# Performance work log

Measured on AMD Instinct MI355X. Metric: run time of the kernel, lower is better.

The kernel has to match this reference:

```python
import jax, jax.numpy as jnp
import numpy as np


def _conv(x, w, b, s):
    # x: NCHW, w: OIHW, VALID padding, stride s
    y = jax.lax.conv_general_dilated(x, w, (s, s), 'VALID',
                                     dimension_numbers=('NCHW', 'OIHW', 'NCHW'))
    return y + b[None, :, None, None]


def _deconv(x, w, b, s):
    # PyTorch ConvTranspose2d (weight IOHW, padding=0): conv of input dilated by s
    # with spatially-flipped, in/out-swapped kernel and full padding k-1.
    k = w.shape[2]
    wk = jnp.flip(w, (2, 3)).transpose(1, 0, 2, 3)  # -> OIHW
    y = jax.lax.conv_general_dilated(x, wk, (1, 1), [(k - 1, k - 1), (k - 1, k - 1)],
                                     lhs_dilation=(s, s),
                                     dimension_numbers=('NCHW', 'OIHW', 'NCHW'))
    return y + b[None, :, None, None]


def setup_inputs() -> dict:
    key = jax.random.key(0)
    ks = iter(jax.random.split(key, 40))
    def p(shape, scale=0.05):
        return jax.random.normal(next(ks), shape, jnp.float32) * scale
    return dict(
        x=jax.random.normal(next(ks), (50, 1, 64, 64), jnp.float32),
        action=jax.random.normal(next(ks), (50, 30), jnp.float32),
        h0=jax.random.normal(next(ks), (50, 1024), jnp.float32),
        c0=jax.random.normal(next(ks), (50, 1024), jnp.float32),
        conv1_w=p((32, 1, 4, 4)), conv1_b=p((32,)),
        conv2_w=p((64, 32, 4, 4)), conv2_b=p((64,)),
        conv3_w=p((128, 64, 4, 4)), conv3_b=p((128,)),
        conv4_w=p((256, 128, 4, 4)), conv4_b=p((256,)),
        fc1_w=p((482, 1024)), fc1_b=p((482,)),
        fc2_w=p((1024, 512)), fc2_b=p((1024,)),
        w_ih=p((4096, 1024)), w_hh=p((4096, 1024)),
        b_ih=p((4096,)), b_hh=p((4096,)),
        fcsd_w=p((1024, 1024)), fcsd_b=p((1024,)),
        d1_w=p((1024, 128, 5, 5)), d1_b=p((128,)),
        d2_w=p((128, 64, 5, 5)), d2_b=p((64,)),
        d3_w=p((64, 32, 6, 6)), d3_b=p((32,)),
        d4_w=p((32, 1, 6, 6)), d4_b=p((1,)),
        fc5_w=p((1, 512)), fc5_b=p((1,)),
    )


def reference(x, action, h0, c0,
              conv1_w, conv1_b, conv2_w, conv2_b, conv3_w, conv3_b, conv4_w, conv4_b,
              fc1_w, fc1_b, fc2_w, fc2_b,
              w_ih, w_hh, b_ih, b_hh,
              fcsd_w, fcsd_b,
              d1_w, d1_b, d2_w, d2_b, d3_w, d3_b, d4_w, d4_b,
              fc5_w, fc5_b):
    B = x.shape[0]  # 50 (hardcoded in original)
    T = 17          # PHYRE_MAX_TIMESTEPS
    h = x
    for w, b in ((conv1_w, conv1_b), (conv2_w, conv2_b), (conv3_w, conv3_b), (conv4_w, conv4_b)):
        h = jnp.tanh(_conv(h, w, b, 2))
    flat = h.reshape(B, -1)                      # [50, 1024]
    fc1 = flat @ fc1_w.T + fc1_b                 # [50, 482]
    z = jnp.concatenate([fc1, action], axis=1)   # [50, 512]
    fc2_out = jax.nn.leaky_relu(z @ fc2_w.T + fc2_b)  # [50, 1024]

    def step(carry, _):
        xt, hs, cs = carry
        g = xt @ w_ih.T + b_ih + hs @ w_hh.T + b_hh   # [B, 4096], gates i,f,g,o
        i, f, gg, o = jnp.split(g, 4, axis=1)
        cs = jax.nn.sigmoid(f) * cs + jax.nn.sigmoid(i) * jnp.tanh(gg)
        hs = jax.nn.sigmoid(o) * jnp.tanh(cs)
        return (hs, hs, cs), hs  # output fed back as next input

    _, outs = jax.lax.scan(step, (fc2_out, h0, c0), None, length=T)  # [17, 50, 1024]
    hd = jax.nn.leaky_relu(jnp.einsum('tbd,ed->tbe', outs, fcsd_w) + fcsd_b)
    hd = hd.reshape(T * B, 1024, 1, 1)  # t-major flatten, matching torch .view
    y = jnp.tanh(_deconv(hd, d1_w, d1_b, 2))   # [850,128,5,5]
    y = jnp.tanh(_deconv(y, d2_w, d2_b, 2))    # [850,64,13,13]
    y = jnp.tanh(_deconv(y, d3_w, d3_b, 2))    # [850,32,30,30]
    y = _deconv(y, d4_w, d4_b, 2)              # [850,1,64,64]
    obs = y.reshape(B, T, 1, 64, 64)  # faithful to original's view (layout quirk)
    reward = z @ fc5_w.T + fc5_b      # [50, 1]
    return obs, reward
```

## Files before the change

### kernel.cpp

```cpp
#include <hip/hip_runtime.h>
#include <math.h>

#define DI __device__ __forceinline__

DI float sigm(float x){ return 1.0f/(1.0f+expf(-x)); }
DI float lrelu(float x){ return x > 0.f ? x : 0.01f*x; }

template<int ACT>
DI float act_apply(float v){
    if (ACT == 1) return tanhf(v);
    if (ACT == 2) return lrelu(v);
    return v;
}

template<int CIN, int COUT>
__global__ __launch_bounds__(256)
void conv_enc_kernel(const float* __restrict__ in, const float* __restrict__ w,
                     const float* __restrict__ bias, float* __restrict__ out,
                     int N, int H, int OH)
{
    int idx = blockIdx.x*256 + threadIdx.x;
    int total = N*COUT*OH*OH;
    if (idx >= total) return;
    int ox = idx % OH; int t = idx / OH;
    int oy = t % OH;   t /= OH;
    int o  = t % COUT; int n = t / COUT;
    float acc = bias[o];
    const float* wp = w + o*CIN*16;
    const float* ip = in + ((size_t)n*CIN)*H*H + (oy*2)*H + ox*2;
    for (int c = 0; c < CIN; ++c) {
        const float* ipc = ip + c*H*H;
        const float* wpc = wp + c*16;
        #pragma unroll
        for (int ky = 0; ky < 4; ++ky)
            #pragma unroll
            for (int kx = 0; kx < 4; ++kx)
                acc = fmaf(ipc[ky*H + kx], wpc[ky*4 + kx], acc);
    }
    out[idx] = tanhf(acc);
}

template<int BM,int BN,int BK,bool BT,int ACT>
__global__ __launch_bounds__((BM/4)*(BN/4))
void gemm_kernel(const float* __restrict__ A, const float* __restrict__ Bm,
                 const float* __restrict__ bias, float* __restrict__ C,
                 int M, int N, int Kfull, int klen, int ldc, int bias_div,
                 long partStride)
{
    constexpr int TM = 4, TN = 4;
    constexpr int THREADS = (BM/TM)*(BN/TN);
    constexpr int LDA = BM + 4, LDB = BN + 4;
    __shared__ __align__(16) float As[BK][LDA];
    __shared__ __align__(16) float Bs[BK][LDB];
    int tid = threadIdx.x;
    int m0 = blockIdx.y * BM, n0 = blockIdx.x * BN;
    int koff = blockIdx.z * klen;
    C += (long)blockIdx.z * partStride;
    constexpr int NTX = BN/TN;
    int tx = tid % NTX, ty = tid / NTX;
    float acc[4][4];
    #pragma unroll
    for (int i=0;i<4;++i)
        #pragma unroll
        for (int j=0;j<4;++j) acc[i][j] = 0.f;

    for (int k0 = 0; k0 < klen; k0 += BK) {
        for (int e = tid; e < BM*BK; e += THREADS) {
            int k = e % BK, m = e / BK;
            As[k][m] = (m0+m < M) ? A[(size_t)(m0+m)*Kfull + koff + k0 + k] : 0.f;
        }
        if (BT) {
            for (int e = tid; e < BN*BK; e += THREADS) {
                int k = e % BK, n = e / BK;
                Bs[k][n] = (n0+n < N) ? Bm[(size_t)(n0+n)*Kfull + koff + k0 + k] : 0.f;
            }
        } else {
            for (int e = tid; e < BN*BK; e += THREADS) {
                int n = e % BN, k = e / BN;
                Bs[k][n] = (n0+n < N) ? Bm[(size_t)(koff + k0 + k)*N + n0+n] : 0.f;
            }
        }
        __syncthreads();
        #pragma unroll 8
        for (int k = 0; k < BK; ++k) {
            float4 a4 = *reinterpret_cast<const float4*>(&As[k][ty*4]);
            float4 b4 = *reinterpret_cast<const float4*>(&Bs[k][tx*4]);
            float av[4] = {a4.x, a4.y, a4.z, a4.w};
            float bv[4] = {b4.x, b4.y, b4.z, b4.w};
            #pragma unroll
            for (int i=0;i<4;++i)
                #pragma unroll
                for (int j=0;j<4;++j)
                    acc[i][j] = fmaf(av[i], bv[j], acc[i][j]);
        }
        __syncthreads();
    }
    #pragma unroll
    for (int i=0;i<4;++i) {
        int m = m0 + ty*4 + i;
        if (m >= M) continue;
        #pragma unroll
        for (int j=0;j<4;++j) {
            int n = n0 + tx*4 + j;
            if (n >= N) continue;
            float v = acc[i][j] + (bias ? bias[n / bias_div] : 0.f);
            C[(size_t)m*ldc + n] = act_apply<ACT>(v);
        }
    }
}

__global__ __launch_bounds__(256)
void addvec_kernel(const float* __restrict__ a, const float* __restrict__ b,
                   float* __restrict__ o, int n)
{
    int i = blockIdx.x*256 + threadIdx.x;
    if (i < n) o[i] = a[i] + b[i];
}

__global__ __launch_bounds__(64)
void concat_action_kernel(const float* __restrict__ action, float* __restrict__ z)
{
    int i = blockIdx.x*64 + threadIdx.x;
    if (i < 50*30) { int b = i/30, k = i%30; z[b*512 + 482 + k] = action[i]; }
}

__global__ __launch_bounds__(64)
void reward_kernel(const float* __restrict__ z, const float* __restrict__ w,
                   const float* __restrict__ b, float* __restrict__ out)
{
    int bi = threadIdx.x;
    if (bi < 50) {
        float acc = b[0];
        for (int k = 0; k < 512; ++k) acc = fmaf(z[bi*512 + k], w[k], acc);
        out[bi] = acc;
    }
}

__global__ __launch_bounds__(256)
void lstm_gates8_kernel(const float* __restrict__ gp, const float* __restrict__ bsum,
                        const float* __restrict__ c_prev,
                        float* __restrict__ c_out, float* __restrict__ h_out,
                        float* __restrict__ outs_t)
{
    int idx = blockIdx.x*256 + threadIdx.x;
    if (idx >= 50*1024) return;
    int b = idx >> 10, j = idx & 1023;
    float s0 = bsum[j], s1 = bsum[1024+j], s2 = bsum[2048+j], s3 = bsum[3072+j];
    #pragma unroll
    for (int p = 0; p < 8; ++p) {
        const float* base = gp + (size_t)p*204800 + b*4096 + j;
        s0 += base[0]; s1 += base[1024]; s2 += base[2048]; s3 += base[3072];
    }
    float cp = c_prev[idx];
    float c = sigm(s1)*cp + sigm(s0)*tanhf(s2);
    float h = sigm(s3)*tanhf(c);
    c_out[idx] = c; h_out[idx] = h; outs_t[idx] = h;
}

__global__ __launch_bounds__(256)
void wprep_kernel(const float* __restrict__ w, float* __restrict__ wp,
                  int CIN, int COUT, int KS)
{
    int idx = blockIdx.x*256 + threadIdx.x;
    int total = 4*CIN*COUT*12;
    if (idx >= total) return;
    int slot = idx % 12; int rem = idx / 12;
    int o = rem % COUT; rem /= COUT;
    int c = rem % CIN;  int pp = rem / CIN;
    int py = pp >> 1, px = pp & 1;
    int j = slot >> 2, i = slot & 3;
    int ky = py + 2*j, kx = px + 2*i;
    float v = 0.f;
    if (i < 3 && ky < KS && kx < KS)
        v = w[(((size_t)c*COUT + o)*KS + ky)*KS + kx];
    wp[idx] = v;
}

template<int CIN,int COUT,int HIN,int HOUT,int ACT,int VSPLIT,int ROWP,int TWU,
         int VPER,int TB,int MWAVES,int ISTR,int OSTR>
__global__ __launch_bounds__(256, MWAVES)
void deconv4_kernel(const float* __restrict__ in, const float* __restrict__ wp,
                    const float* __restrict__ bias, float* __restrict__ out)
{
    constexpr int NV = (HOUT + 1) / 2;
    constexpr int NVSEG = (NV + VSPLIT - 1) / VSPLIT;
    constexpr int NVB = (NVSEG + VPER - 1) / VPER;
    constexpr int ROWS_MAX = (NVSEG + 2 < HIN) ? (NVSEG + 2) : HIN;
    constexpr int NR4 = (TWU + 2 + 3) / 4;
    constexpr int RLEN = (TWU == 1) ? 4 : NR4*4;
    static_assert(NVB * COUT * TB <= 256, "tasks must fit one per thread");
    __shared__ __align__(16) float slab[CIN*ROWS_MAX*ROWP];

    int n   = blockIdx.x / VSPLIT;
    int seg = blockIdx.x % VSPLIT;
    int v0 = seg * NVSEG;
    int v1 = (v0 + NVSEG < NV) ? v0 + NVSEG : NV;
    int r0 = (v0 - 2 > 0) ? v0 - 2 : 0;
    int r1m = (v1 - 1 < HIN - 1) ? v1 - 1 : HIN - 1;
    int nrows = r1m - r0 + 1;
    int tid = threadIdx.x;
    const float* inb = in + (size_t)n*CIN*HIN*ISTR;
    const size_t PPSTR = (size_t)CIN*COUT*12;

    for (int e = tid; e < CIN*ROWS_MAX; e += 256) {
        int c = e / ROWS_MAX, ri = e % ROWS_MAX;
        if (ri < nrows) {
            const float* src = inb + ((size_t)c*HIN + r0 + ri)*ISTR;
            float* dst = slab + (c*ROWS_MAX + ri)*ROWP;
            dst[0] = 0.f; dst[1] = 0.f;
            #pragma unroll
            for (int x2 = HIN+2; x2 < ROWP; ++x2) dst[x2] = 0.f;
            for (int x2 = 0; x2 < HIN; ++x2) dst[2+x2] = src[x2];
        }
    }
    __syncthreads();

    int task = tid;
    int vi = task % NVB; int rem = task / NVB;
    int o = rem % COUT;  int tb = rem / COUT;
    int u0 = tb * TWU;
    bool anyv = false;
    int vg[VPER];
    #pragma unroll
    for (int q = 0; q < VPER; ++q) {
        vg[q] = v0 + vi + q*NVB;
        if (vg[q] < v1) anyv = true;
    }
    if (tb >= TB) anyv = false;

    float acc[VPER][2][2][TWU];
    #pragma unroll
    for (int q=0;q<VPER;++q)
        #pragma unroll
        for (int a=0;a<2;++a)
            #pragma unroll
            for (int b=0;b<2;++b)
                #pragma unroll
                for (int t=0;t<TWU;++t) acc[q][a][b][t] = 0.f;

    if (anyv) {
        const float* wb0 = wp + (size_t)o*12;
        for (int c = 0; c < CIN; ++c) {
            const float* wbase = wb0 + (size_t)c*COUT*12;
            const float* sc = slab + c*(ROWS_MAX*ROWP);
            #pragma unroll
            for (int jj = 0; jj < 3; ++jj) {
                float r[VPER][RLEN];
                #pragma unroll
                for (int q = 0; q < VPER; ++q) {
                    int iy = vg[q] - jj;
                    if (iy >= 0 && iy < HIN) {
                        const float* srow = sc + (iy - r0)*ROWP + u0;
                        if constexpr (TWU == 1) {
                            r[q][0] = srow[0]; r[q][1] = srow[1]; r[q][2] = srow[2];
                        } else {
                            #pragma unroll
                            for (int p4 = 0; p4 < NR4; ++p4) {
                                float4 f = *reinterpret_cast<const float4*>(srow + p4*4);
                                r[q][p4*4]=f.x; r[q][p4*4+1]=f.y; r[q][p4*4+2]=f.z; r[q][p4*4+3]=f.w;
                            }
                        }
                    } else {
                        #pragma unroll
                        for (int p4 = 0; p4 < RLEN; ++p4) r[q][p4] = 0.f;
                    }
                }
                #pragma unroll
                for (int pp = 0; pp < 4; ++pp) {
                    float4 w4 = *reinterpret_cast<const float4*>(wbase + pp*PPSTR + jj*4);
                    int py = pp >> 1, px = pp & 1;
                    #pragma unroll
                    for (int q = 0; q < VPER; ++q)
                        #pragma unroll
                        for (int t = 0; t < TWU; ++t)
                            acc[q][py][px][t] =
                                fmaf(w4.x, r[q][t+2],
                                fmaf(w4.y, r[q][t+1],
                                fmaf(w4.z, r[q][t], acc[q][py][px][t])));
                }
            }
        }
        float bv = bias[o];
        #pragma unroll
        for (int q = 0; q < VPER; ++q) {
            if (vg[q] >= v1) continue;
            #pragma unroll
            for (int py = 0; py < 2; ++py) {
                int y = py + 2*vg[q];
                if (y >= HOUT) continue;
                float* ob = out + (((size_t)n*COUT + o)*HOUT + y)*OSTR;
                #pragma unroll
                for (int t = 0; t < TWU; ++t) {
                    int x0 = 2*(u0+t);
                    if (x0 + 1 < HOUT) {
                        float2 qv;
                        qv.x = act_apply<ACT>(acc[q][py][0][t] + bv);
                        qv.y = act_apply<ACT>(acc[q][py][1][t] + bv);
                        *reinterpret_cast<float2*>(ob + x0) = qv;
                    } else if (x0 < HOUT) {
                        ob[x0] = act_apply<ACT>(acc[q][py][0][t] + bv);
                    }
                }
            }
        }
    }
}

extern "C" void kernel_launch(void* const* d_in, const int* in_sizes, int n_in,
                              void* d_out, int out_size, void* d_ws, size_t ws_size,
                              hipStream_t stream)
{
    const float* x       = (const float*)d_in[0];
    const float* action  = (const float*)d_in[1];
    const float* h0      = (const float*)d_in[2];
    const float* c0      = (const float*)d_in[3];
    const float* conv1_w = (const float*)d_in[4];  const float* conv1_b = (const float*)d_in[5];
    const float* conv2_w = (const float*)d_in[6];  const float* conv2_b = (const float*)d_in[7];
    const float* conv3_w = (const float*)d_in[8];  const float* conv3_b = (const float*)d_in[9];
    const float* conv4_w = (const float*)d_in[10]; const float* conv4_b = (const float*)d_in[11];
    const float* fc1_w   = (const float*)d_in[12]; const float* fc1_b   = (const float*)d_in[13];
    const float* fc2_w   = (const float*)d_in[14]; const float* fc2_b   = (const float*)d_in[15];
    const float* w_ih    = (const float*)d_in[16]; const float* w_hh    = (const float*)d_in[17];
    const float* b_ih    = (const float*)d_in[18]; const float* b_hh    = (const float*)d_in[19];
    const float* fcsd_w  = (const float*)d_in[20]; const float* fcsd_b  = (const float*)d_in[21];
    const float* d1_w    = (const float*)d_in[22]; const float* d1_b    = (const float*)d_in[23];
    const float* d2_w    = (const float*)d_in[24]; const float* d2_b    = (const float*)d_in[25];
    const float* d3_w    = (const float*)d_in[26]; const float* d3_b    = (const float*)d_in[27];
    const float* d4_w    = (const float*)d_in[28]; const float* d4_b    = (const float*)d_in[29];
    const float* fc5_w   = (const float*)d_in[30]; const float* fc5_b   = (const float*)d_in[31];
    float* out = (float*)d_out;
    float* ws  = (float*)d_ws;

    float* a1   = ws;
    float* a2   = a1 + 1537600;
    float* a3   = a2 + 627200;
    float* flat = a3 + 230400;
    float* z    = flat + 51200;
    float* fc2o = z + 25600;
    float* hbuf = fc2o + 51200;
    float* cbuf = hbuf + 51200;
    float* outs = cbuf + 51200;
    float* hd   = outs + 870400;
    float* wsum = hd + 870400;
    float* bsum = wsum + 4194304;
    float* wp2  = bsum + 4096;
    float* wp3  = wp2 + 393216;
    float* wp4  = wp3 + 98304;
    float* y1   = wp4 + 1536;
    float* y2   = y1 + 2720000;
    float* y3   = y2 + 11315200;
    float* g8   = y1;

    const int B = 50;
    const long GP = 204800;

    addvec_kernel<<<(4194304+255)/256, 256, 0, stream>>>(w_ih, w_hh, wsum, 4194304);
    addvec_kernel<<<(4096+255)/256, 256, 0, stream>>>(b_ih, b_hh, bsum, 4096);
    wprep_kernel<<<(4*128*64*12+255)/256, 256, 0, stream>>>(d2_w, wp2, 128, 64, 5);
    wprep_kernel<<<(4*64*32*12+255)/256, 256, 0, stream>>>(d3_w, wp3, 64, 32, 6);
    wprep_kernel<<<(4*32*1*12+255)/256, 256, 0, stream>>>(d4_w, wp4, 32, 1, 6);

    conv_enc_kernel<1,32><<<(B*32*31*31+255)/256, 256, 0, stream>>>(x, conv1_w, conv1_b, a1, B, 64, 31);
    conv_enc_kernel<32,64><<<(B*64*14*14+255)/256, 256, 0, stream>>>(a1, conv2_w, conv2_b, a2, B, 31, 14);
    conv_enc_kernel<64,128><<<(B*128*6*6+255)/256, 256, 0, stream>>>(a2, conv3_w, conv3_b, a3, B, 14, 6);
    conv_enc_kernel<128,256><<<(B*256*2*2+255)/256, 256, 0, stream>>>(a3, conv4_w, conv4_b, flat, B, 6, 2);

    {
        dim3 grid((482+63)/64, (B+31)/32, 1);
        gemm_kernel<32,64,32,true,0><<<grid, 128, 0, stream>>>(flat, fc1_w, fc1_b, z, B, 482, 1024, 1024, 512, 1, 0);
    }
    concat_action_kernel<<<(1500+63)/64, 64, 0, stream>>>(action, z);
    reward_kernel<<<1, 64, 0, stream>>>(z, fc5_w, fc5_b, out + (size_t)850*4096);

    {
        dim3 grid((1024+63)/64, (B+31)/32, 1);
        gemm_kernel<32,64,32,true,2><<<grid, 128, 0, stream>>>(z, fc2_w, fc2_b, fc2o, B, 1024, 512, 512, 1024, 1, 0);
    }

    {
        dim3 grid0(64, 2, 4);
        gemm_kernel<32,64,32,true,0><<<grid0, 128, 0, stream>>>(fc2o, w_ih, nullptr, g8, B, 4096, 1024, 256, 4096, 1, GP);
        gemm_kernel<32,64,32,true,0><<<grid0, 128, 0, stream>>>(h0, w_hh, nullptr, g8 + 4*GP, B, 4096, 1024, 256, 4096, 1, GP);
        lstm_gates8_kernel<<<200, 256, 0, stream>>>(g8, bsum, c0, cbuf, hbuf, outs);
        dim3 gridt(64, 2, 8);
        for (int t = 1; t < 17; ++t) {
            gemm_kernel<32,64,32,true,0><<<gridt, 128, 0, stream>>>(hbuf, wsum, nullptr, g8, B, 4096, 1024, 128, 4096, 1, GP);
            lstm_gates8_kernel<<<200, 256, 0, stream>>>(g8, bsum, cbuf, cbuf, hbuf, outs + (size_t)t*51200);
        }
    }

    {
        dim3 grid((1024+63)/64, (850+63)/64, 1);
        gemm_kernel<64,64,32,true,2><<<grid, 256, 0, stream>>>(outs, fcsd_w, fcsd_b, hd, 850, 1024, 1024, 1024, 1024, 1, 0);
    }
    {
        dim3 grid((3200+63)/64, (850+63)/64, 1);
        gemm_kernel<64,64,32,false,1><<<grid, 256, 0, stream>>>(hd, d1_w, d1_b, y1, 850, 3200, 1024, 1024, 3200, 25, 0);
    }

    deconv4_kernel<128,64,5,13,1, 1,12,7,2,1,3, 5,16><<<850, 256, 0, stream>>>(y1, wp2, d2_b, y2);
    deconv4_kernel<64,32,13,30,1, 2,20,8,2,2,3, 16,32><<<1700, 256, 0, stream>>>(y2, wp3, d3_b, y3);
    deconv4_kernel<32,1,30,64,0, 4,36,1,1,32,3, 32,64><<<3400, 256, 0, stream>>>(y3, wp4, d4_b, out);

    (void)in_sizes; (void)n_in; (void)out_size; (void)ws_size;
}
```

Measured before the change: 3.448 ms.

## Fuse LSTM recurrence into persistent cooperative kernel with LDS-resident weights

Replaces the per-timestep GEMM plus gate kernel launches with a single cooperative kernel of 256 blocks. Each block keeps its 16 rows of w_ih+w_hh in LDS and applies the gates locally, with a grid-wide sync between steps. This removes about 34 launches and the repeated reads of the 16MB summed weight matrix, but the hidden state now flows through transposed global buffers and grid.sync. The diff also retunes the deconv template parameters to exact output sizes, which changes workspace layout.

```diff
diff --git a/kernel.cpp b/kernel.cpp
--- a/kernel.cpp
+++ b/kernel.cpp
@@ -1,5 +1,8 @@
 #include <hip/hip_runtime.h>
+#include <hip/hip_cooperative_groups.h>
 #include <math.h>
+
+namespace cg = cooperative_groups;
 
 #define DI __device__ __forceinline__
 
@@ -109,14 +112,6 @@
     }
 }
 
-__global__ __launch_bounds__(256)
-void addvec_kernel(const float* __restrict__ a, const float* __restrict__ b,
-                   float* __restrict__ o, int n)
-{
-    int i = blockIdx.x*256 + threadIdx.x;
-    if (i < n) o[i] = a[i] + b[i];
-}
-
 __global__ __launch_bounds__(64)
 void concat_action_kernel(const float* __restrict__ action, float* __restrict__ z)
 {
@@ -137,24 +132,107 @@
 }
 
 __global__ __launch_bounds__(256)
-void lstm_gates8_kernel(const float* __restrict__ gp, const float* __restrict__ bsum,
-                        const float* __restrict__ c_prev,
-                        float* __restrict__ c_out, float* __restrict__ h_out,
-                        float* __restrict__ outs_t)
+void transpose_bt_kernel(const float* __restrict__ in, float* __restrict__ out)
 {
     int idx = blockIdx.x*256 + threadIdx.x;
-    if (idx >= 50*1024) return;
-    int b = idx >> 10, j = idx & 1023;
-    float s0 = bsum[j], s1 = bsum[1024+j], s2 = bsum[2048+j], s3 = bsum[3072+j];
-    #pragma unroll
-    for (int p = 0; p < 8; ++p) {
-        const float* base = gp + (size_t)p*204800 + b*4096 + j;
-        s0 += base[0]; s1 += base[1024]; s2 += base[2048]; s3 += base[3072];
-    }
-    float cp = c_prev[idx];
-    float c = sigm(s1)*cp + sigm(s0)*tanhf(s2);
-    float h = sigm(s3)*tanhf(c);
-    c_out[idx] = c; h_out[idx] = h; outs_t[idx] = h;
+    if (idx >= 1024*64) return;
+    int j = idx >> 6, b = idx & 63;
+    out[idx] = (b < 50) ? in[(size_t)b*1024 + j] : 0.f;
+}
+
+__global__ __launch_bounds__(256)
+void lstm_coop_kernel(const float* __restrict__ fc2oT, const float* __restrict__ h0T,
+                      const float* __restrict__ c0,
+                      const float* __restrict__ w_ih, const float* __restrict__ w_hh,
+                      const float* __restrict__ b_ih, const float* __restrict__ b_hh,
+                      float* __restrict__ hTbuf, float* __restrict__ outs)
+{
+    constexpr int LDW = 1025;
+    __shared__ float wlds[16*LDW];
+    __shared__ float gbuf[16][64];
+    __shared__ float cst[4][52];
+    __shared__ float ldsb[16];
+    const int blk = blockIdx.x;
+    const int tid = threadIdx.x;
+
+    for (int e = tid; e < 16*1024; e += 256) {
+        int jcol = e >> 10, k = e & 1023;
+        int row = 4*blk + (jcol & 3) + 1024*(jcol >> 2);
+        wlds[jcol*LDW + k] = w_ih[(size_t)row*1024 + k] + w_hh[(size_t)row*1024 + k];
+    }
+    if (tid < 16) {
+        int row = 4*blk + (tid & 3) + 1024*(tid >> 2);
+        ldsb[tid] = b_ih[row] + b_hh[row];
+    }
+    if (tid < 200) {
+        int ci = tid & 3, b = tid >> 2;
+        cst[ci][b] = c0[(size_t)b*1024 + 4*blk + ci];
+    }
+
+    cg::grid_group grid = cg::this_grid();
+
+    const int jp = tid >> 5;
+    const int bg = tid & 31;
+    const int jc0 = jp, jc1 = jp + 8;
+    const int row0 = 4*blk + (jc0 & 3) + 1024*(jc0 >> 2);
+    const int row1 = 4*blk + (jc1 & 3) + 1024*(jc1 >> 2);
+
+    for (int t = 0; t < 17; ++t) {
+        float a00 = 0.f, a01 = 0.f, a10 = 0.f, a11 = 0.f;
+        if (t == 0) {
+            const float* wa = w_ih + (size_t)row0*1024;
+            const float* wb = w_ih + (size_t)row1*1024;
+            #pragma unroll 4
+            for (int k = 0; k < 1024; ++k) {
+                float x0 = fc2oT[k*64 + bg];
+                float x1 = fc2oT[k*64 + bg + 32];
+                float w0 = wa[k], w1 = wb[k];
+                a00 = fmaf(w0, x0, a00); a01 = fmaf(w0, x1, a01);
+                a10 = fmaf(w1, x0, a10); a11 = fmaf(w1, x1, a11);
+            }
+            wa = w_hh + (size_t)row0*1024;
+            wb = w_hh + (size_t)row1*1024;
+            #pragma unroll 4
+            for (int k = 0; k < 1024; ++k) {
+                float x0 = h0T[k*64 + bg];
+                float x1 = h0T[k*64 + bg + 32];
+                float w0 = wa[k], w1 = wb[k];
+                a00 = fmaf(w0, x0, a00); a01 = fmaf(w0, x1, a01);
+                a10 = fmaf(w1, x0, a10); a11 = fmaf(w1, x1, a11);
+            }
+        } else {
+            const float* hTr = hTbuf + (size_t)(t & 1)*65536;
+            const float* wa = wlds + jc0*LDW;
+            const float* wb = wlds + jc1*LDW;
+            #pragma unroll 4
+            for (int k = 0; k < 1024; ++k) {
+                float x0 = hTr[k*64 + bg];
+                float x1 = hTr[k*64 + bg + 32];
+                float w0 = wa[k], w1 = wb[k];
+                a00 = fmaf(w0, x0, a00); a01 = fmaf(w0, x1, a01);
+                a10 = fmaf(w1, x0, a10); a11 = fmaf(w1, x1, a11);
+            }
+        }
+        gbuf[jc0][bg] = a00; gbuf[jc0][bg+32] = a01;
+        gbuf[jc1][bg] = a10; gbuf[jc1][bg+32] = a11;
+        __syncthreads();
+        if (tid < 200) {
+            int ci = tid & 3, b = tid >> 2;
+            float gi = gbuf[ci][b]      + ldsb[ci];
+            float gf = gbuf[4+ci][b]    + ldsb[4+ci];
+            float gg = gbuf[8+ci][b]    + ldsb[8+ci];
+            float go = gbuf[12+ci][b]   + ldsb[12+ci];
+            float c = sigm(gf)*cst[ci][b] + sigm(gi)*tanhf(gg);
+            float h = sigm(go)*tanhf(c);
+            cst[ci][b] = c;
+            int col = 4*blk + ci;
+            float* hTw = hTbuf + (size_t)((t + 1) & 1)*65536;
+            hTw[(size_t)col*64 + b] = h;
+            outs[(size_t)t*51200 + (size_t)b*1024 + col] = h;
+        }
+        if (t < 16) { __threadfence(); grid.sync(); }
+        else        { __syncthreads(); }
+    }
 }
 
 __global__ __launch_bounds__(256)
@@ -331,31 +409,26 @@
     float* out = (float*)d_out;
     float* ws  = (float*)d_ws;
 
-    float* a1   = ws;
-    float* a2   = a1 + 1537600;
-    float* a3   = a2 + 627200;
-    float* flat = a3 + 230400;
-    float* z    = flat + 51200;
-    float* fc2o = z + 25600;
-    float* hbuf = fc2o + 51200;
-    float* cbuf = hbuf + 51200;
-    float* outs = cbuf + 51200;
-    float* hd   = outs + 870400;
-    float* wsum = hd + 870400;
-    float* bsum = wsum + 4194304;
-    float* wp2  = bsum + 4096;
-    float* wp3  = wp2 + 393216;
-    float* wp4  = wp3 + 98304;
-    float* y1   = wp4 + 1536;
-    float* y2   = y1 + 2720000;
-    float* y3   = y2 + 11315200;
-    float* g8   = y1;
+    float* a1    = ws;
+    float* a2    = a1 + 1537600;
+    float* a3    = a2 + 627200;
+    float* flat  = a3 + 230400;
+    float* z     = flat + 51200;
+    float* fc2o  = z + 25600;
+    float* outs  = fc2o + 51200;
+    float* hd    = outs + 870400;
+    float* wp2   = hd + 870400;
+    float* wp3   = wp2 + 393216;
+    float* wp4   = wp3 + 98304;
+    float* y1    = wp4 + 1536;
+    float* y2    = y1 + 2720000;
+    float* y3    = y2 + 9193600;
+    float* fc2oT = y3 + 24480000;
+    float* h0T   = fc2oT + 65536;
+    float* hTbuf = h0T + 65536;
 
     const int B = 50;
-    const long GP = 204800;
-
-    addvec_kernel<<<(4194304+255)/256, 256, 0, stream>>>(w_ih, w_hh, wsum, 4194304);
-    addvec_kernel<<<(4096+255)/256, 256, 0, stream>>>(b_ih, b_hh, bsum, 4096);
+
     wprep_kernel<<<(4*128*64*12+255)/256, 256, 0, stream>>>(d2_w, wp2, 128, 64, 5);
     wprep_kernel<<<(4*64*32*12+255)/256, 256, 0, stream>>>(d3_w, wp3, 64, 32, 6);
     wprep_kernel<<<(4*32*1*12+255)/256, 256, 0, stream>>>(d4_w, wp4, 32, 1, 6);
@@ -377,16 +450,14 @@
         gemm_kernel<32,64,32,true,2><<<grid, 128, 0, stream>>>(z, fc2_w, fc2_b, fc2o, B, 1024, 512, 512, 1024, 1, 0);
     }
 
+    transpose_bt_kernel<<<(65536+255)/256, 256, 0, stream>>>(fc2o, fc2oT);
+    transpose_bt_kernel<<<(65536+255)/256, 256, 0, stream>>>(h0, h0T);
     {
-        dim3 grid0(64, 2, 4);
-        gemm_kernel<32,64,32,true,0><<<grid0, 128, 0, stream>>>(fc2o, w_ih, nullptr, g8, B, 4096, 1024, 256, 4096, 1, GP);
-        gemm_kernel<32,64,32,true,0><<<grid0, 128, 0, stream>>>(h0, w_hh, nullptr, g8 + 4*GP, B, 4096, 1024, 256, 4096, 1, GP);
-        lstm_gates8_kernel<<<200, 256, 0, stream>>>(g8, bsum, c0, cbuf, hbuf, outs);
-        dim3 gridt(64, 2, 8);
-        for (int t = 1; t < 17; ++t) {
-            gemm_kernel<32,64,32,true,0><<<gridt, 128, 0, stream>>>(hbuf, wsum, nullptr, g8, B, 4096, 1024, 128, 4096, 1, GP);
-            lstm_gates8_kernel<<<200, 256, 0, stream>>>(g8, bsum, cbuf, cbuf, hbuf, outs + (size_t)t*51200);
-        }
+        void* kargs[] = { (void*)&fc2oT, (void*)&h0T, (void*)&c0,
+                          (void*)&w_ih, (void*)&w_hh, (void*)&b_ih, (void*)&b_hh,
+                          (void*)&hTbuf, (void*)&outs };
+        hipLaunchCooperativeKernel((const void*)lstm_coop_kernel,
+                                   dim3(256), dim3(256), kargs, 0, stream);
     }
 
     {
@@ -398,9 +469,9 @@
         gemm_kernel<64,64,32,false,1><<<grid, 256, 0, stream>>>(hd, d1_w, d1_b, y1, 850, 3200, 1024, 1024, 3200, 25, 0);
     }
 
-    deconv4_kernel<128,64,5,13,1, 1,12,7,2,1,3, 5,16><<<850, 256, 0, stream>>>(y1, wp2, d2_b, y2);
-    deconv4_kernel<64,32,13,30,1, 2,20,8,2,2,3, 16,32><<<1700, 256, 0, stream>>>(y2, wp3, d3_b, y3);
-    deconv4_kernel<32,1,30,64,0, 4,36,1,1,32,3, 32,64><<<3400, 256, 0, stream>>>(y3, wp4, d4_b, out);
+    deconv4_kernel<128,64,5,13,1, 1,12,7,2,1,3, 5,13><<<850, 256, 0, stream>>>(y1, wp2, d2_b, y2);
+    deconv4_kernel<64,32,13,30,1, 2,20,15,1,1,3, 13,30><<<1700, 256, 0, stream>>>(y2, wp3, d3_b, y3);
+    deconv4_kernel<32,1,30,64,0, 4,36,1,1,32,3, 30,64><<<3400, 256, 0, stream>>>(y3, wp4, d4_b, out);
 
     (void)in_sizes; (void)n_in; (void)out_size; (void)ws_size;
 }
```

Result: slower. 4.650 ms (+34.9%).
